# Optimization experiments

Measured on AMD Instinct MI355X. Metric: run time of the kernel, lower is better.

The kernel has to match this reference:

```python
import jax, jax.numpy as jnp
from jax import lax
import numpy as np

EPS = 1e-7  # keras.backend.epsilon()
DISCOUNT = 1.0

B, T, S, F = 32, 128, 64, 256  # samples, sentences, steps, features


def setup_inputs() -> dict:
    key = jax.random.key(0)
    ks = jax.random.split(key, 6)
    scale = 1.0 / np.sqrt(F)
    return {
        "x": jax.random.normal(ks[0], (B, T, S, F), dtype=jnp.float32),
        "W": jax.random.normal(ks[1], (F, F), dtype=jnp.float32) * scale,
        "W_context": jax.random.normal(ks[2], (F, F), dtype=jnp.float32) * scale,
        "W_l": jax.random.normal(ks[3], (F,), dtype=jnp.float32) * scale,
        "W_lc": jax.random.normal(ks[4], (F,), dtype=jnp.float32) * scale,
        "bl": jnp.zeros((1,), dtype=jnp.float32),
        "b": jnp.zeros((F,), dtype=jnp.float32),
        "u": jax.random.normal(ks[5], (F,), dtype=jnp.float32) * scale,
    }


def _forward(x, W, W_context, W_l, W_lc, bl, b, u):
    # x: [B, T, S, F]; scan over sentence axis T with carried context [B, F].
    def step(carry, x_):
        context, count = carry            # context: [B, F]
        context_ = context                # aggregate == 'sum'
        uit = jnp.einsum("bsf,fg->bsg", x_, W)            # [B, S, F]
        c = context_ @ W_context                            # [B, F]
        # gate: l = sigmoid(<context, W_lc> + bl broadcast over steps + <x, W_l>)
        gate_logit = (context_ @ W_lc + bl[0])[:, None] + x_ @ W_l  # [B, S]
        l = jax.nn.sigmoid(gate_logit)[..., None]           # [B, S, 1]
        uit = jnp.tanh(l * uit + (1.0 - l) * c[:, None, :] + b)
        ait = uit @ u                                        # [B, S]
        a = jnp.exp(ait)
        a = a / (jnp.sum(a, axis=1, keepdims=True) + EPS)   # masked-softmax (no mask)
        attended = jnp.einsum("bsf,bs->bf", x_, a)          # [B, F]
        new_context = context * DISCOUNT + attended
        return (new_context, count + 1.0), (attended, a, new_context)

    x_t = jnp.transpose(x, (1, 0, 2, 3))  # [T, B, S, F]
    init = (jnp.zeros((x.shape[0], x.shape[-1]), x.dtype), jnp.asarray(0.0, x.dtype))
    _, (out, weights, ctx) = lax.scan(step, init, x_t)
    output = jnp.transpose(out, (1, 0, 2))       # [B, T, F]
    context = jnp.transpose(ctx, (1, 0, 2))      # [B, T, F]
    weights = jnp.transpose(weights, (1, 0, 2))  # [B, T, S]
    return output, context, weights


def reference(x, W, W_context, W_l, W_lc, bl, b, u):
    return _forward(x, W, W_context, W_l, W_lc, bl, b, u)
```

## Files before the change

kernel.cpp:

```cpp
#include <hip/hip_runtime.h>
#include <stdint.h>

#define Tdim 128
#define Bdim 32
#define Sdim 64
#define Fdim 256

typedef unsigned short u16;
typedef short bf16x8 __attribute__((ext_vector_type(8)));
typedef float f32x4 __attribute__((ext_vector_type(4)));

#define K2     2.8853900817779268f
#define LOG2E  1.4426950408889634f

__device__ __forceinline__ u16 f2b(float f){
  union { float f; uint32_t u; } v; v.f = f;
  uint32_t u = v.u;
  if ((u & 0x7fffffffu) > 0x7f800000u) return (u16)0x7fc0;
  uint32_t r = (u + 0x7fffu + ((u >> 16) & 1u)) >> 16;
  return (u16)r;
}
__device__ __forceinline__ float b2f(u16 h){
  union { uint32_t u; float f; } v; v.u = ((uint32_t)h) << 16; return v.f;
}
__device__ __forceinline__ float b2f_lo(uint32_t w){
  union { uint32_t u; float f; } v; v.u = w << 16; return v.f;
}
__device__ __forceinline__ float b2f_hi(uint32_t w){
  union { uint32_t u; float f; } v; v.u = w & 0xffff0000u; return v.f;
}
__device__ __forceinline__ uint32_t pack2(float a, float b){
  return (uint32_t)f2b(a) | ((uint32_t)f2b(b) << 16);
}
__device__ __forceinline__ uint4 pack8(const float4 a, const float4 b){
  uint4 r;
  r.x = pack2(a.x, a.y); r.y = pack2(a.z, a.w);
  r.z = pack2(b.x, b.y); r.w = pack2(b.z, b.w);
  return r;
}


__global__ __launch_bounds__(256) void kt_transpose_cvt(const float* __restrict__ Wg,
                                                        u16* __restrict__ Wt){
  __shared__ u16 tile[64*66];
  int bx = blockIdx.x;
  int ti = bx >> 2, tj = bx & 3;
  int t = threadIdx.x;
#pragma unroll
  for (int i = 0; i < 16; ++i){
    int e = t*16 + i;
    int r = e >> 6, c = e & 63;
    tile[r*66 + c] = f2b(Wg[(ti*64 + r)*256 + tj*64 + c]);
  }
  __syncthreads();
#pragma unroll
  for (int i = 0; i < 16; ++i){
    int e = t*16 + i;
    int r = e >> 6, c = e & 63;
    Wt[(tj*64 + r)*256 + ti*64 + c] = tile[c*66 + r];
  }
}

__global__ __launch_bounds__(256) void kt_gemm(const float* __restrict__ Xg,
                                               const u16* __restrict__ Wt,
                                               const float* __restrict__ Wlg,
                                               u16* __restrict__ Pg,
                                               float* __restrict__ qg){
  __shared__ u16 Ws[128*72];
  __shared__ u16 Xs[128*72];
  __shared__ float Wls[256];
  int t  = threadIdx.x;
  int bx = blockIdx.x;
  int mt = bx >> 1, nt = bx & 1;
  int r0 = mt*128, g0 = nt*128;
  Wls[t & 255] = Wlg[t & 255];
  int lane = t & 63, wv = t >> 6;
  int goff = (wv & 1)*64, roff = (wv >> 1)*64;
  int fr = lane & 15, fq = lane >> 4;
  f32x4 acc[4][4];
#pragma unroll
  for (int a = 0; a < 4; ++a)
#pragma unroll
    for (int b = 0; b < 4; ++b)
      acc[a][b] = (f32x4){0.f,0.f,0.f,0.f};
  float qacc = 0.f;

  for (int kk = 0; kk < 4; ++kk){
    int k0 = kk*64;
    __syncthreads();
#pragma unroll
    for (int uu = 0; uu < 4; ++uu){
      int unit = uu*256 + t;
      int row = unit >> 3, c = unit & 7;
      *(uint4*)&Ws[row*72 + c*8] = *(const uint4*)&Wt[(g0+row)*256 + k0 + c*8];
      const float4* xp = (const float4*)&Xg[(size_t)(r0+row)*256 + k0 + c*8];
      *(uint4*)&Xs[row*72 + c*8] = pack8(xp[0], xp[1]);
    }
    __syncthreads();
    if (nt == 0 && t < 128){
      int r = t;
#pragma unroll
      for (int c = 0; c < 8; ++c){
        uint4 xv = *(const uint4*)&Xs[r*72 + c*8];
        const uint32_t* xw = (const uint32_t*)&xv;
#pragma unroll
        for (int p = 0; p < 4; ++p){
          qacc = fmaf(b2f_lo(xw[p]), Wls[k0 + c*8 + 2*p],     qacc);
          qacc = fmaf(b2f_hi(xw[p]), Wls[k0 + c*8 + 2*p + 1], qacc);
        }
      }
    }
#pragma unroll
    for (int ks = 0; ks < 64; ks += 32){
      bf16x8 af[4], bf_[4];
#pragma unroll
      for (int mi = 0; mi < 4; ++mi)
        af[mi] = *(const bf16x8*)&Ws[(goff + mi*16 + fr)*72 + ks + fq*8];
#pragma unroll
      for (int ni = 0; ni < 4; ++ni)
        bf_[ni] = *(const bf16x8*)&Xs[(roff + ni*16 + fr)*72 + ks + fq*8];
#pragma unroll
      for (int mi = 0; mi < 4; ++mi)
#pragma unroll
        for (int ni = 0; ni < 4; ++ni)
          acc[mi][ni] = __builtin_amdgcn_mfma_f32_16x16x32_bf16(
              af[mi], bf_[ni], acc[mi][ni], 0, 0, 0);
    }
  }
#pragma unroll
  for (int mi = 0; mi < 4; ++mi){
    int g = g0 + goff + mi*16 + fq*4;
    int grp = g >> 4;
#pragma unroll
    for (int ni = 0; ni < 4; ++ni){
      int r = r0 + roff + ni*16 + fr;
      int bt = r >> 6, s = r & 63;
      ushort4 st;
      st.x = f2b(acc[mi][ni][0]); st.y = f2b(acc[mi][ni][1]);
      st.z = f2b(acc[mi][ni][2]); st.w = f2b(acc[mi][ni][3]);
      *(ushort4*)&Pg[(size_t)bt*16384 + grp*1024 + s*16 + fq*4] = st;
    }
  }
  if (nt == 0 && t < 128) qg[r0 + t] = qacc;
}

__global__ __launch_bounds__(1024, 4) void kt_scan5(
    const float* __restrict__ Xg, const u16* __restrict__ Pf,
    const float* __restrict__ qf, const float* __restrict__ Wcg,
    const float* __restrict__ Wlcg, const float* __restrict__ blg,
    const float* __restrict__ biasg, const float* __restrict__ ug,
    float* __restrict__ out)
{
  __shared__ float ctx_s[256], bbr_s[256], ur_s[256], wlc_s[256];
  __shared__ float pp[64*17];
  __shared__ float attp[16*260];
  __shared__ float glc_p[4];

  const int tid   = threadIdx.x;
  const int b     = blockIdx.x;
  const int lane  = tid & 63;
  const int wave  = tid >> 6;
  const int g_loc = lane >> 2;
  const int fc    = lane & 3;
  const int gcol  = wave*16 + g_loc;
  const int f     = tid & 255;

  uint32_t wcp2[32];
#pragma unroll
  for (int i = 0; i < 16; ++i){
    int m  = (4*fc + i) & 15;
    int fb = fc*64 + m*4;
    wcp2[2*i]   = pack2(Wcg[(fb+0)*256 + gcol], Wcg[(fb+1)*256 + gcol]);
    wcp2[2*i+1] = pack2(Wcg[(fb+2)*256 + gcol], Wcg[(fb+3)*256 + gcol]);
  }

  if (tid < 256){
    ctx_s[tid] = 0.f;
    bbr_s[tid] = K2 * biasg[tid];
    ur_s[tid]  = ug[tid];
    wlc_s[tid] = Wlcg[tid];
  }
  if (tid < 4) glc_p[tid] = 0.f;
  const float blf = blg[0];
  float glcr = 0.f;

  const u16*    pP = Pf + (size_t)(b*Tdim)*16384 + wave*1024 + lane*16;
  const float4* pX = (const float4*)Xg + (size_t)(b*Tdim)*4096 + wave*256 + lane;
  const float*  pq = qf + (size_t)(b*Tdim)*64 + lane;

  uint32_t pw[8];
  {
    const uint4* pp_ = (const uint4*)pP;
    *(uint4*)&pw[0] = pp_[0]; *(uint4*)&pw[4] = pp_[1];
  }
  float qcur = pq[0];

  float* outO = out;
  float* outC = out + Bdim*Tdim*Fdim;
  float* outW = out + 2*Bdim*Tdim*Fdim;
  __syncthreads();

  for (int tt = 0; tt < Tdim; ++tt){
    const int bt    = b*Tdim + tt;
    const int nstep = (tt < Tdim-1) ? 1 : 0;

    uint32_t pwn[8];
    {
      const uint4* pp_ = (const uint4*)(pP + (size_t)nstep*16384);
      *(uint4*)&pwn[0] = pp_[0]; *(uint4*)&pwn[4] = pp_[1];
    }
    float qn = pq[nstep*64];
    float4 x0 = pX[0], x1 = pX[64], x2 = pX[128], x3 = pX[192];

    {
      glcr += glc_p[0] + glc_p[1] + glc_p[2] + glc_p[3];
      float logit = glcr + blf + qcur;
      float sig = __builtin_amdgcn_rcpf(1.f + __builtin_exp2f(-LOG2E*logit));
      const float l2  = K2 * sig;
      const float l2b = K2 - K2*sig;

      float pa = 0.f;
#pragma unroll
      for (int i = 0; i < 16; ++i){
        int m = (4*fc + i) & 15;
        float4 cv = *(const float4*)&ctx_s[fc*64 + m*4];
        pa = fmaf(cv.x, b2f_lo(wcp2[2*i]),   pa);
        pa = fmaf(cv.y, b2f_hi(wcp2[2*i]),   pa);
        pa = fmaf(cv.z, b2f_lo(wcp2[2*i+1]), pa);
        pa = fmaf(cv.w, b2f_hi(wcp2[2*i+1]), pa);
      }
      pa += __shfl_xor(pa, 1, 64);
      pa += __shfl_xor(pa, 2, 64);
      float c[16];
#pragma unroll
      for (int j = 0; j < 16; ++j)
        c[j] = __shfl(pa, 4*j, 64);

      float ait = 0.f;
#pragma unroll
      for (int j = 0; j < 16; ++j){
        float pv = (j & 1) ? b2f_hi(pw[j>>1]) : b2f_lo(pw[j>>1]);
        float bb = bbr_s[wave*16 + j];
        float uu = ur_s[wave*16 + j];
        float z  = fmaf(l2, pv, fmaf(l2b, c[j], bb));
        float e  = __builtin_exp2f(z);
        float r  = __builtin_amdgcn_rcpf(e + 1.f);
        ait += fmaf(-2.f*uu, r, uu);
      }
      pp[lane*17 + wave] = ait;
    }
    __syncthreads();

    {
      const int ppb = lane*17;
      float ait = 0.f;
#pragma unroll
      for (int k = 0; k < 16; ++k) ait += pp[ppb + k];
      float mx = ait;
#pragma unroll
      for (int off = 32; off > 0; off >>= 1)
        mx = fmaxf(mx, __shfl_xor(mx, off, 64));
      float e = __builtin_exp2f(LOG2E*(ait - mx));
      float ssum = e;
#pragma unroll
      for (int off = 32; off > 0; off >>= 1)
        ssum += __shfl_xor(ssum, off, 64);
      float denom = ssum + 1e-7f * __builtin_exp2f(-LOG2E*mx);
      float a = e * __builtin_amdgcn_rcpf(denom);
      if (wave == 0) outW[(size_t)bt*Sdim + lane] = a;

      const float av0 = __shfl(a, wave*4 + 0, 64);
      const float av1 = __shfl(a, wave*4 + 1, 64);
      const float av2 = __shfl(a, wave*4 + 2, 64);
      const float av3 = __shfl(a, wave*4 + 3, 64);
      float4 acc;
      acc.x = av0*x0.x; acc.y = av0*x0.y; acc.z = av0*x0.z; acc.w = av0*x0.w;
      acc.x = fmaf(av1, x1.x, acc.x); acc.y = fmaf(av1, x1.y, acc.y);
      acc.z = fmaf(av1, x1.z, acc.z); acc.w = fmaf(av1, x1.w, acc.w);
      acc.x = fmaf(av2, x2.x, acc.x); acc.y = fmaf(av2, x2.y, acc.y);
      acc.z = fmaf(av2, x2.z, acc.z); acc.w = fmaf(av2, x2.w, acc.w);
      acc.x = fmaf(av3, x3.x, acc.x); acc.y = fmaf(av3, x3.y, acc.y);
      acc.z = fmaf(av3, x3.z, acc.z); acc.w = fmaf(av3, x3.w, acc.w);
      *(float4*)&attp[wave*260 + lane*4] = acc;
    }
    __syncthreads();

    if (tid < 256){
      float att = 0.f;
#pragma unroll
      for (int k = 0; k < 16; ++k) att += attp[k*260 + f];
      const size_t o = (size_t)bt*Fdim + f;
      outO[o] = att;
      float nc = ctx_s[f] + att;
      ctx_s[f] = nc;
      outC[o] = nc;
      float gp = att * wlc_s[f];
#pragma unroll
      for (int off = 32; off > 0; off >>= 1)
        gp += __shfl_xor(gp, off, 64);
      if (lane == 0) glc_p[wave] = gp;
    }
    __syncthreads();

#pragma unroll
    for (int k = 0; k < 8; ++k) pw[k] = pwn[k];
    qcur = qn;
    pP += (size_t)nstep*16384;
    pX += 4096;
    pq += 64;
  }
}

__global__ __launch_bounds__(1024) void fused_ctx_attn(
    const float* __restrict__ Xg, const float* __restrict__ Wg,
    const float* __restrict__ Wcg, const float* __restrict__ Wlg,
    const float* __restrict__ Wlcg, const float* __restrict__ blg,
    const float* __restrict__ biasg, const float* __restrict__ ug,
    float* __restrict__ out)
{
  __shared__ u16   xs[64*272];
  __shared__ float ps[64*257];
  __shared__ float cpart[8*258];
  __shared__ float qp[64*5];
  __shared__ float pp[64*17];
  __shared__ float attp[4*260];
  __shared__ float ctx_s[256], c_s[256], bb_s[256], u_s[256], wlc_s[256], wl_s[256];
  __shared__ float l2_s[64], l2b_s[64], a_s[64];
  __shared__ float glc_p[4];

  const int tid  = threadIdx.x;
  const int b    = blockIdx.x;
  const int lane = tid & 63;
  const int wave = tid >> 6;
  const int fr   = lane & 15;
  const int fq   = lane >> 4;
  const int f    = tid & 255;
  const int sb   = tid >> 8;

  bf16x8 afW[8];
  {
    const int gcol = wave*16 + fr;
#pragma unroll
    for (int kt = 0; kt < 8; ++kt){
      u16 tmp[8];
#pragma unroll
      for (int j = 0; j < 8; ++j)
        tmp[j] = f2b(Wg[(kt*32 + fq*8 + j)*256 + gcol]);
      afW[kt] = *(const bf16x8*)tmp;
    }
  }
  const int fj = tid >> 7;
  const int gp = tid & 127;
  uint32_t wcp[32];
#pragma unroll
  for (int fi = 0; fi < 32; ++fi)
    wcp[fi] = pack2(Wcg[(fj*32 + fi)*256 + gp*2], Wcg[(fj*32 + fi)*256 + gp*2 + 1]);

  if (tid < 256){
    ctx_s[tid] = 0.f;
    bb_s[tid]  = K2 * biasg[tid];
    u_s[tid]   = ug[tid];
    wlc_s[tid] = Wlcg[tid];
    wl_s[tid]  = Wlg[tid];
  }
  if (tid < 4) glc_p[tid] = 0.f;
  const float blf = blg[0];
  float glcr = 0.f;

  float* outO = out;
  float* outC = out + Bdim*Tdim*Fdim;
  float* outW = out + 2*Bdim*Tdim*Fdim;

  const int srow = tid >> 5;
  const int sc8  = (tid & 31)*8;
  {
    const long xb = (long)(b*Tdim)*Sdim*Fdim;
    const float4* p0 = (const float4*)&Xg[xb + (long)srow*256 + sc8];
    const float4* p1 = (const float4*)&Xg[xb + (long)(srow+32)*256 + sc8];
    *(uint4*)&xs[srow*272 + sc8]      = pack8(p0[0], p0[1]);
    *(uint4*)&xs[(srow+32)*272 + sc8] = pack8(p1[0], p1[1]);
  }
  __syncthreads();

  for (int tt = 0; tt < Tdim; ++tt){
    const int tn = (tt < Tdim-1) ? (tt+1) : tt;
    const long xb = (long)((b*Tdim + tn))*Sdim*Fdim;
    const float4* p0 = (const float4*)&Xg[xb + (long)srow*256 + sc8];
    const float4* p1 = (const float4*)&Xg[xb + (long)(srow+32)*256 + sc8];
    uint4 xr0 = pack8(p0[0], p0[1]);
    uint4 xr1 = pack8(p1[0], p1[1]);

    {
      float pa = 0.f, pb = 0.f;
#pragma unroll
      for (int fi = 0; fi < 32; ++fi){
        float cf = ctx_s[fj*32 + fi];
        pa = fmaf(cf, b2f_lo(wcp[fi]), pa);
        pb = fmaf(cf, b2f_hi(wcp[fi]), pb);
      }
      float2 st; st.x = pa; st.y = pb;
      *(float2*)&cpart[fj*258 + gp*2] = st;
    }
    {
      f32x4 acc[4];
#pragma unroll
      for (int nt = 0; nt < 4; ++nt) acc[nt] = (f32x4){0.f,0.f,0.f,0.f};
#pragma unroll
      for (int kt = 0; kt < 8; ++kt){
#pragma unroll
        for (int nt = 0; nt < 4; ++nt){
          bf16x8 bfx = *(const bf16x8*)&xs[(nt*16 + fr)*272 + kt*32 + fq*8];
          acc[nt] = __builtin_amdgcn_mfma_f32_16x16x32_bf16(afW[kt], bfx, acc[nt], 0, 0, 0);
        }
      }
#pragma unroll
      for (int nt = 0; nt < 4; ++nt){
        const int s = nt*16 + fr;
        const int g = wave*16 + fq*4;
        ps[s*257 + g + 0] = acc[nt][0];
        ps[s*257 + g + 1] = acc[nt][1];
        ps[s*257 + g + 2] = acc[nt][2];
        ps[s*257 + g + 3] = acc[nt][3];
      }
    }
    if (tid < 256){
      const int s = tid >> 2, qtr = tid & 3;
      float a = 0.f;
#pragma unroll
      for (int j = 0; j < 64; ++j)
        a = fmaf(b2f(xs[s*272 + qtr*64 + j]), wl_s[qtr*64 + j], a);
      qp[s*5 + qtr] = a;
    }
    __syncthreads();

    if (tid < 256){
      float a = 0.f;
#pragma unroll
      for (int k = 0; k < 8; ++k) a += cpart[k*258 + tid];
      c_s[tid] = a;
    }
    if (tid < 64){
      glcr += glc_p[0] + glc_p[1] + glc_p[2] + glc_p[3];
      float q = qp[tid*5] + qp[tid*5+1] + qp[tid*5+2] + qp[tid*5+3];
      float logit = glcr + blf + q;
      float sig = 1.f / (1.f + __builtin_exp2f(-LOG2E*logit));
      l2_s[tid]  = K2 * sig;
      l2b_s[tid] = K2 - K2*sig;
    }
    __syncthreads();

    {
      const float cf = c_s[f], bbf = bb_s[f], uf = u_s[f], n2 = -2.f*u_s[f];
#pragma unroll
      for (int i = 0; i < 16; ++i){
        const int s = sb*16 + i;
        float z2 = fmaf(l2_s[s], ps[s*257 + f], fmaf(l2b_s[s], cf, bbf));
        float e  = __builtin_exp2f(z2);
        float r  = 1.f / (e + 1.f);
        ps[s*257 + f] = fmaf(n2, r, uf);
      }
    }
    __syncthreads();

    {
      const int s = tid & 63, grp = tid >> 6;
      float a = 0.f;
#pragma unroll
      for (int k = 0; k < 16; ++k) a += ps[s*257 + grp*16 + k];
      pp[s*17 + grp] = a;
    }
    __syncthreads();

    if (tid < 64){
      const int s = tid;
      float ait = 0.f;
#pragma unroll
      for (int k = 0; k < 16; ++k) ait += pp[s*17 + k];
      float m = ait;
#pragma unroll
      for (int off = 32; off > 0; off >>= 1)
        m = fmaxf(m, __shfl_xor(m, off, 64));
      float e = __builtin_exp2f(LOG2E*(ait - m));
      float ssum = e;
#pragma unroll
      for (int off = 32; off > 0; off >>= 1)
        ssum += __shfl_xor(ssum, off, 64);
      float denom = ssum + 1e-7f * __builtin_exp2f(-LOG2E*m);
      float a = e / denom;
      a_s[s] = a;
      outW[(b*Tdim + tt)*Sdim + s] = a;
    }
    __syncthreads();

    {
      float ap = 0.f;
#pragma unroll
      for (int i = 0; i < 16; ++i){
        const int s = sb*16 + i;
        ap = fmaf(a_s[s], b2f(xs[s*272 + f]), ap);
      }
      attp[sb*260 + f] = ap;
    }
    __syncthreads();

    if (tid < 256){
      float att = attp[f] + attp[260+f] + attp[520+f] + attp[780+f];
      const int o = (b*Tdim + tt)*Fdim + f;
      outO[o] = att;
      float nc = ctx_s[f] + att;
      ctx_s[f] = nc;
      outC[o] = nc;
      float gpart = att * wlc_s[f];
#pragma unroll
      for (int off = 32; off > 0; off >>= 1)
        gpart += __shfl_xor(gpart, off, 64);
      if (lane == 0) glc_p[wave] = gpart;
    }
    *(uint4*)&xs[srow*272 + sc8] = xr0;
    *(uint4*)&xs[(srow+32)*272 + sc8] = xr1;
    __syncthreads();
  }
}

extern "C" void kernel_launch(void* const* d_in, const int* in_sizes, int n_in,
                              void* d_out, int out_size, void* d_ws, size_t ws_size,
                              hipStream_t stream){
  const float* x    = (const float*)d_in[0];
  const float* W    = (const float*)d_in[1];
  const float* Wc   = (const float*)d_in[2];
  const float* Wl   = (const float*)d_in[3];
  const float* Wlc  = (const float*)d_in[4];
  const float* bl   = (const float*)d_in[5];
  const float* bias = (const float*)d_in[6];
  const float* u    = (const float*)d_in[7];
  float* out = (float*)d_out;

  const size_t P_BYTES  = (size_t)4096*16384*2;
  const size_t Q_BYTES  = (size_t)262144*4;
  const size_t WT_BYTES = (size_t)256*256*2;
  const size_t NEED = P_BYTES + Q_BYTES + WT_BYTES;

  if (ws_size >= NEED){
    uint8_t* ws = (uint8_t*)d_ws;
    u16*   P  = (u16*)ws;
    float* q  = (float*)(ws + P_BYTES);
    u16*   Wt = (u16*)(ws + P_BYTES + Q_BYTES);
    kt_transpose_cvt<<<16, 256, 0, stream>>>(W, Wt);
    kt_gemm<<<4096, 256, 0, stream>>>(x, Wt, Wl, P, q);
    kt_scan5<<<Bdim, 1024, 0, stream>>>(x, P, q, Wc, Wlc, bl, bias, u, out);
  } else {
    fused_ctx_attn<<<Bdim, 1024, 0, stream>>>(x, W, Wc, Wl, Wlc, bl, bias, u, out);
  }
}
```

Before: 1.082 ms.

## Widen GEMM tile to full N and use lighter LDS-only barriers in scan

The projection GEMM now has each 512-thread block compute all 256 output columns for a 128-row tile, instead of splitting N across two blocks. Each x tile is therefore loaded from global memory and converted to bf16 only once, and the Wl dot product is no longer skewed toward half the blocks. In the sequential scan kernel, the three __syncthreads are replaced by a custom barrier that waits only on LDS counters before s_barrier. That cuts per-step barrier overhead on the serial critical path, at the cost of relying on no pending global loads needing to complete across the barrier. The larger block uses more LDS and registers per block, which may lower occupancy.

```diff
diff --git a/kernel.cpp b/kernel.cpp
--- a/kernel.cpp
+++ b/kernel.cpp
@@ -39,6 +39,12 @@
   return r;
 }
 
+__device__ __forceinline__ void bar_lds(){
+  asm volatile("s_waitcnt lgkmcnt(0)" ::: "memory");
+  __builtin_amdgcn_s_barrier();
+  asm volatile("" ::: "memory");
+}
+
 
 __global__ __launch_bounds__(256) void kt_transpose_cvt(const float* __restrict__ Wg,
                                                         u16* __restrict__ Wt){
@@ -61,21 +67,19 @@
   }
 }
 
-__global__ __launch_bounds__(256) void kt_gemm(const float* __restrict__ Xg,
-                                               const u16* __restrict__ Wt,
-                                               const float* __restrict__ Wlg,
-                                               u16* __restrict__ Pg,
-                                               float* __restrict__ qg){
-  __shared__ u16 Ws[128*72];
+__global__ __launch_bounds__(512, 4) void kt_gemm2(const float* __restrict__ Xg,
+                                                   const u16* __restrict__ Wt,
+                                                   const float* __restrict__ Wlg,
+                                                   u16* __restrict__ Pg,
+                                                   float* __restrict__ qg){
+  __shared__ u16 Ws[256*72];
   __shared__ u16 Xs[128*72];
   __shared__ float Wls[256];
   int t  = threadIdx.x;
-  int bx = blockIdx.x;
-  int mt = bx >> 1, nt = bx & 1;
-  int r0 = mt*128, g0 = nt*128;
-  Wls[t & 255] = Wlg[t & 255];
+  int r0 = blockIdx.x * 128;
+  if (t < 256) Wls[t] = Wlg[t];
   int lane = t & 63, wv = t >> 6;
-  int goff = (wv & 1)*64, roff = (wv >> 1)*64;
+  int goff = (wv & 3)*64, roff = (wv >> 2)*64;
   int fr = lane & 15, fq = lane >> 4;
   f32x4 acc[4][4];
 #pragma unroll
@@ -90,14 +94,19 @@
     __syncthreads();
 #pragma unroll
     for (int uu = 0; uu < 4; ++uu){
-      int unit = uu*256 + t;
+      int unit = uu*512 + t;
       int row = unit >> 3, c = unit & 7;
-      *(uint4*)&Ws[row*72 + c*8] = *(const uint4*)&Wt[(g0+row)*256 + k0 + c*8];
+      *(uint4*)&Ws[row*72 + c*8] = *(const uint4*)&Wt[row*256 + k0 + c*8];
+    }
+#pragma unroll
+    for (int uu = 0; uu < 2; ++uu){
+      int unit = uu*512 + t;
+      int row = unit >> 3, c = unit & 7;
       const float4* xp = (const float4*)&Xg[(size_t)(r0+row)*256 + k0 + c*8];
       *(uint4*)&Xs[row*72 + c*8] = pack8(xp[0], xp[1]);
     }
     __syncthreads();
-    if (nt == 0 && t < 128){
+    if (t < 128){
       int r = t;
 #pragma unroll
       for (int c = 0; c < 8; ++c){
@@ -129,7 +138,7 @@
   }
 #pragma unroll
   for (int mi = 0; mi < 4; ++mi){
-    int g = g0 + goff + mi*16 + fq*4;
+    int g = goff + mi*16 + fq*4;
     int grp = g >> 4;
 #pragma unroll
     for (int ni = 0; ni < 4; ++ni){
@@ -141,10 +150,10 @@
       *(ushort4*)&Pg[(size_t)bt*16384 + grp*1024 + s*16 + fq*4] = st;
     }
   }
-  if (nt == 0 && t < 128) qg[r0 + t] = qacc;
-}
-
-__global__ __launch_bounds__(1024, 4) void kt_scan5(
+  if (t < 128) qg[r0 + t] = qacc;
+}
+
+__global__ __launch_bounds__(1024, 4) void kt_scan6(
     const float* __restrict__ Xg, const u16* __restrict__ Pf,
     const float* __restrict__ qf, const float* __restrict__ Wcg,
     const float* __restrict__ Wlcg, const float* __restrict__ blg,
@@ -249,7 +258,7 @@
       }
       pp[lane*17 + wave] = ait;
     }
-    __syncthreads();
+    bar_lds();
 
     {
       const int ppb = lane*17;
@@ -283,7 +292,7 @@
       acc.z = fmaf(av3, x3.z, acc.z); acc.w = fmaf(av3, x3.w, acc.w);
       *(float4*)&attp[wave*260 + lane*4] = acc;
     }
-    __syncthreads();
+    bar_lds();
 
     if (tid < 256){
       float att = 0.f;
@@ -300,7 +309,7 @@
         gp += __shfl_xor(gp, off, 64);
       if (lane == 0) glc_p[wave] = gp;
     }
-    __syncthreads();
+    bar_lds();
 
 #pragma unroll
     for (int k = 0; k < 8; ++k) pw[k] = pwn[k];
@@ -546,8 +555,8 @@
     float* q  = (float*)(ws + P_BYTES);
     u16*   Wt = (u16*)(ws + P_BYTES + Q_BYTES);
     kt_transpose_cvt<<<16, 256, 0, stream>>>(W, Wt);
-    kt_gemm<<<4096, 256, 0, stream>>>(x, Wt, Wl, P, q);
-    kt_scan5<<<Bdim, 1024, 0, stream>>>(x, P, q, Wc, Wlc, bl, bias, u, out);
+    kt_gemm2<<<2048, 512, 0, stream>>>(x, Wt, Wl, P, q);
+    kt_scan6<<<Bdim, 1024, 0, stream>>>(x, P, q, Wc, Wlc, bl, bias, u, out);
   } else {
     fused_ctx_attn<<<Bdim, 1024, 0, stream>>>(x, W, Wc, Wl, Wlc, bl, bias, u, out);
   }
```

Result: no change. 1.082 ms (+0.0%).
